# Performance work log

Measured on AMD Instinct MI355X. Metric: run time of the kernel, lower is better.

## Reference

```python
import jax, jax.numpy as jnp
import numpy as np

CUTOFFS = [20000, 40000, 200000, 267735]
CUTOFF_ENDS = [0] + CUTOFFS
DIMS = [1024, 256, 64, 16]  # d_embed // div_val**i


def setup_inputs() -> dict:
    key = jax.random.key(0)
    ks = jax.random.split(key, 20)
    def rn(k, shape):
        return jax.random.normal(k, shape, dtype=jnp.float32) * 0.02
    inp = {}
    inp["hidden"] = jax.random.normal(ks[0], (64, 8, 1024), dtype=jnp.float32)
    inp["target"] = jax.random.randint(ks[1], (64, 8), 0, 267735)
    inp["cluster_weight"] = rn(ks[2], (3, 1024))
    inp["cluster_bias"] = jnp.zeros((3,), jnp.float32)
    for i in range(4):
        n = CUTOFF_ENDS[i + 1] - CUTOFF_ENDS[i]
        inp[f"W{i}"] = rn(ks[3 + 3 * i], (n, DIMS[i]))
        inp[f"b{i}"] = jnp.zeros((n,), jnp.float32)
        inp[f"P{i}"] = rn(ks[4 + 3 * i], (DIMS[i], 1024))
    return inp


def _logit(h, W, b, P):
    # h: [s, b, d_proj]; P: [d_emb_i, d_proj]; W: [n_i, d_emb_i]
    y = jnp.einsum('ibd,ed->ibe', h, P)
    return jnp.einsum('ibe,ne->ibn', y, W) + b


def reference(hidden, target, cluster_weight, cluster_bias,
              W0, b0, P0, W1, b1, P1, W2, b2, P2, W3, b3, P3):
    Ws = [W0, W1, W2, W3]
    bs = [b0, b1, b2, b3]
    Ps = [P0, P1, P2, P3]

    # head cluster: real head tokens + cluster logits appended
    head_W = jnp.concatenate([W0, cluster_weight], axis=0)   # [20003, 1024]
    head_b = jnp.concatenate([b0, cluster_bias], axis=0)
    head_lp = jax.nn.log_softmax(_logit(hidden, head_W, head_b, P0), axis=-1)

    outs = [head_lp[..., :CUTOFFS[0]]]
    loss = jnp.zeros(target.shape, jnp.float32)

    mask = (target >= 0) & (target < CUTOFFS[0])
    ct = jnp.clip(target, 0, CUTOFFS[0] - 1)
    cur = jnp.take_along_axis(head_lp, ct[..., None], axis=-1)[..., 0]
    loss = jnp.where(mask, cur, loss)

    for i in range(1, 4):
        l_idx, r_idx = CUTOFF_ENDS[i], CUTOFF_ENDS[i + 1]
        tail_lp = jax.nn.log_softmax(_logit(hidden, Ws[i], bs[i], Ps[i]), axis=-1)
        # joint log-prob = cluster log-prob + within-cluster log-prob
        lp_i = head_lp[..., CUTOFFS[0] + i - 1, None] + tail_lp
        outs.append(lp_i)
        mask = (target >= l_idx) & (target < r_idx)
        ct = jnp.clip(target - l_idx, 0, r_idx - l_idx - 1)
        cur = jnp.take_along_axis(lp_i, ct[..., None], axis=-1)[..., 0]
        loss = jnp.where(mask, cur, loss)

    out = jnp.concatenate(outs, axis=-1)  # [s, b, vocab]
    loss = jnp.mean(-loss)                # return_mean=True
    return out, loss
```

## Files before the change

### kernel.cpp

```cpp
#include <hip/hip_runtime.h>


typedef __bf16 bf16x8 __attribute__((ext_vector_type(8)));
typedef float  f32x4  __attribute__((ext_vector_type(4)));

#define NEG_HUGE (-3.402823466e38f)

__device__ __forceinline__ unsigned short f2bf(float x) {
  unsigned int u = __float_as_uint(x);
  u = (u + 0x7fffu + ((u >> 16) & 1u)) >> 16;
  return (unsigned short)u;
}
__device__ __forceinline__ float bf2f(unsigned short h) {
  return __uint_as_float(((unsigned int)h) << 16);
}
__device__ __forceinline__ void mergeMS(float& m, float& s, float mo, float so) {
  float mn = fmaxf(m, mo);
  s = s * __expf(m - mn) + so * __expf(mo - mn);
  m = mn;
}

__global__ __launch_bounds__(256) void convert_h_kernel(
    const float* __restrict__ h, unsigned short* __restrict__ o) {
  int i = (blockIdx.x * 256 + threadIdx.x) * 4;
  float4 v = *reinterpret_cast<const float4*>(h + i);
  uint2 u;
  u.x = (unsigned int)f2bf(v.x) | ((unsigned int)f2bf(v.y) << 16);
  u.y = (unsigned int)f2bf(v.z) | ((unsigned int)f2bf(v.w) << 16);
  *reinterpret_cast<uint2*>(o + i) = u;
}

struct CvtDesc {
  const float* src[7];
  unsigned short* dst[7];
  int n4[7];
  int blk0[8];
};

__global__ __launch_bounds__(256) void convert_w_kernel(CvtDesc d) {
  int b = blockIdx.x, seg = 0;
  while (seg < 6 && b >= d.blk0[seg + 1]) ++seg;
  const float* __restrict__ s = d.src[seg];
  unsigned short* __restrict__ o = d.dst[seg];
  const int n4 = d.n4[seg];
  int base = (b - d.blk0[seg]) * 1024 + threadIdx.x;
#pragma unroll
  for (int i = 0; i < 4; ++i) {
    int v = base + i * 256;
    if (v < n4) {
      float4 x = reinterpret_cast<const float4*>(s)[v];
      uint2 u;
      u.x = (unsigned int)f2bf(x.x) | ((unsigned int)f2bf(x.y) << 16);
      u.y = (unsigned int)f2bf(x.z) | ((unsigned int)f2bf(x.w) << 16);
      reinterpret_cast<uint2*>(o)[v] = u;
    }
  }
}

__global__ __launch_bounds__(256) void convert_w3_kernel(
    const float* __restrict__ s, unsigned short* __restrict__ o) {
  int t = blockIdx.x * 256 + threadIdx.x;
  int row = t >> 2, j = t & 3;
  if (row >= 67735) return;
  uint4 u = make_uint4(0u, 0u, 0u, 0u);
  if (j < 2) {
    float4 a = reinterpret_cast<const float4*>(s)[row * 4 + j * 2];
    float4 b = reinterpret_cast<const float4*>(s)[row * 4 + j * 2 + 1];
    u.x = (unsigned int)f2bf(a.x) | ((unsigned int)f2bf(a.y) << 16);
    u.y = (unsigned int)f2bf(a.z) | ((unsigned int)f2bf(a.w) << 16);
    u.z = (unsigned int)f2bf(b.x) | ((unsigned int)f2bf(b.y) << 16);
    u.w = (unsigned int)f2bf(b.z) | ((unsigned int)f2bf(b.w) << 16);
  }
  reinterpret_cast<uint4*>(o)[row * 4 + j] = u;
}

template <bool SOFTMAX>
__global__ __launch_bounds__(256) void gemm_reg_kernel(
    const unsigned short* __restrict__ A, int lda, int K,
    const unsigned short* __restrict__ Bh, int ldb,
    const float* __restrict__ bias, int N,
    float* __restrict__ outF, long long ldo,
    unsigned short* __restrict__ outH, int ldh,
    float* __restrict__ partials, int nChunks) {
  __shared__ float red[64][4][2];
  const int tid = threadIdx.x;
  const int lane = tid & 63, w = tid >> 6;
  const int q = lane >> 4, l15 = lane & 15;
  const int row0 = blockIdx.x * 64;
  const int colBase = blockIdx.y * 256;

  const char* Ac = (const char*)A;
  const char* Bc = (const char*)Bh;
  int colg[4];
  unsigned aoff[4], boff[4];
#pragma unroll
  for (int nb = 0; nb < 4; ++nb) {
    colg[nb] = colBase + w * 64 + nb * 16 + l15;
    int cl = colg[nb] < N ? colg[nb] : N - 1;
    boff[nb] = (unsigned)((cl * ldb + q * 8) * 2);
  }
#pragma unroll
  for (int mb = 0; mb < 4; ++mb)
    aoff[mb] = (unsigned)(((row0 + mb * 16 + l15) * lda + q * 8) * 2);

  f32x4 acc[4][4];
#pragma unroll
  for (int i = 0; i < 4; ++i)
#pragma unroll
    for (int j = 0; j < 4; ++j) acc[i][j] = (f32x4){0.f, 0.f, 0.f, 0.f};

  for (int k = 0; k < K; k += 32) {
    bf16x8 fa[4], fb[4];
#pragma unroll
    for (int mb = 0; mb < 4; ++mb)
      fa[mb] = *reinterpret_cast<const bf16x8*>(Ac + aoff[mb] + 2 * k);
#pragma unroll
    for (int nb = 0; nb < 4; ++nb)
      fb[nb] = *reinterpret_cast<const bf16x8*>(Bc + boff[nb] + 2 * k);
#pragma unroll
    for (int mb = 0; mb < 4; ++mb)
#pragma unroll
      for (int nb = 0; nb < 4; ++nb)
        acc[mb][nb] = __builtin_amdgcn_mfma_f32_16x16x32_bf16(
            fa[mb], fb[nb], acc[mb][nb], 0, 0, 0);
  }

  if (SOFTMAX) {
    float bv[4];
#pragma unroll
    for (int nb = 0; nb < 4; ++nb) bv[nb] = (colg[nb] < N) ? bias[colg[nb]] : 0.f;
#pragma unroll
    for (int mb = 0; mb < 4; ++mb)
#pragma unroll
      for (int nb = 0; nb < 4; ++nb)
#pragma unroll
        for (int r = 0; r < 4; ++r) acc[mb][nb][r] += bv[nb];
#pragma unroll
    for (int mb = 0; mb < 4; ++mb)
#pragma unroll
      for (int nb = 0; nb < 4; ++nb)
        if (colg[nb] < N) {
#pragma unroll
          for (int r = 0; r < 4; ++r) {
            int rowg = row0 + mb * 16 + q * 4 + r;
            outF[(size_t)rowg * ldo + colg[nb]] = acc[mb][nb][r];
          }
        }
#pragma unroll
    for (int mb = 0; mb < 4; ++mb) {
#pragma unroll
      for (int r = 0; r < 4; ++r) {
        float mx = NEG_HUGE, s = 0.f;
#pragma unroll
        for (int nb = 0; nb < 4; ++nb)
          if (colg[nb] < N) mx = fmaxf(mx, acc[mb][nb][r]);
#pragma unroll
        for (int nb = 0; nb < 4; ++nb)
          if (colg[nb] < N) s += __expf(acc[mb][nb][r] - mx);
        for (int off = 1; off < 16; off <<= 1) {
          float mo = __shfl_xor(mx, off);
          float so = __shfl_xor(s, off);
          mergeMS(mx, s, mo, so);
        }
        if (l15 == 0) {
          red[mb * 16 + q * 4 + r][w][0] = mx;
          red[mb * 16 + q * 4 + r][w][1] = s;
        }
      }
    }
    __syncthreads();
    if (tid < 64) {
      float m = red[tid][0][0], s = red[tid][0][1];
#pragma unroll
      for (int ww = 1; ww < 4; ++ww) mergeMS(m, s, red[tid][ww][0], red[tid][ww][1]);
      size_t pi = ((size_t)(row0 + tid) * nChunks + blockIdx.y) * 2;
      partials[pi] = m;
      partials[pi + 1] = s;
    }
  } else {
#pragma unroll
    for (int mb = 0; mb < 4; ++mb)
#pragma unroll
      for (int nb = 0; nb < 4; ++nb)
        if (colg[nb] < ldh) {
#pragma unroll
          for (int r = 0; r < 4; ++r) {
            int rowg = row0 + mb * 16 + q * 4 + r;
            outH[(size_t)rowg * ldh + colg[nb]] =
                (colg[nb] < N) ? f2bf(acc[mb][nb][r]) : (unsigned short)0;
          }
        }
  }
}

template <int KS>
__global__ __launch_bounds__(256) void gemm_reg_mloop_kernel(
    const unsigned short* __restrict__ A, int lda,
    const unsigned short* __restrict__ Bh, int ldb,
    const float* __restrict__ bias, int N,
    float* __restrict__ outF, long long ldo,
    float* __restrict__ partials, int nChunks) {
  __shared__ float red[64][4][2];
  const int tid = threadIdx.x;
  const int lane = tid & 63, w = tid >> 6;
  const int q = lane >> 4, l15 = lane & 15;
  const int colBase = blockIdx.x * 256;

  const char* Ac = (const char*)A;
  const char* Bc = (const char*)Bh;
  int colg[4];
  float bv[4];
  bf16x8 fbr[KS][4];
#pragma unroll
  for (int nb = 0; nb < 4; ++nb) {
    colg[nb] = colBase + w * 64 + nb * 16 + l15;
    int cl = colg[nb] < N ? colg[nb] : N - 1;
    bv[nb] = (colg[nb] < N) ? bias[colg[nb]] : 0.f;
#pragma unroll
    for (int s = 0; s < KS; ++s)
      fbr[s][nb] = *reinterpret_cast<const bf16x8*>(
          Bc + (size_t)((cl * ldb + s * 32 + q * 8) * 2));
  }

  for (int m = 0; m < 8; ++m) {
    const int row0 = m * 64;
    f32x4 acc[4][4];
#pragma unroll
    for (int i = 0; i < 4; ++i)
#pragma unroll
      for (int j = 0; j < 4; ++j) acc[i][j] = (f32x4){0.f, 0.f, 0.f, 0.f};
#pragma unroll
    for (int s = 0; s < KS; ++s) {
      bf16x8 fa[4];
#pragma unroll
      for (int mb = 0; mb < 4; ++mb)
        fa[mb] = *reinterpret_cast<const bf16x8*>(
            Ac + (size_t)(((row0 + mb * 16 + l15) * lda + s * 32 + q * 8) * 2));
#pragma unroll
      for (int mb = 0; mb < 4; ++mb)
#pragma unroll
        for (int nb = 0; nb < 4; ++nb)
          acc[mb][nb] = __builtin_amdgcn_mfma_f32_16x16x32_bf16(
              fa[mb], fbr[s][nb], acc[mb][nb], 0, 0, 0);
    }
#pragma unroll
    for (int mb = 0; mb < 4; ++mb)
#pragma unroll
      for (int nb = 0; nb < 4; ++nb)
#pragma unroll
        for (int r = 0; r < 4; ++r) acc[mb][nb][r] += bv[nb];
#pragma unroll
    for (int mb = 0; mb < 4; ++mb)
#pragma unroll
      for (int nb = 0; nb < 4; ++nb)
        if (colg[nb] < N) {
#pragma unroll
          for (int r = 0; r < 4; ++r) {
            int rowg = row0 + mb * 16 + q * 4 + r;
            outF[(size_t)rowg * ldo + colg[nb]] = acc[mb][nb][r];
          }
        }
#pragma unroll
    for (int mb = 0; mb < 4; ++mb) {
#pragma unroll
      for (int r = 0; r < 4; ++r) {
        float mx = NEG_HUGE, s = 0.f;
#pragma unroll
        for (int nb = 0; nb < 4; ++nb)
          if (colg[nb] < N) mx = fmaxf(mx, acc[mb][nb][r]);
#pragma unroll
        for (int nb = 0; nb < 4; ++nb)
          if (colg[nb] < N) s += __expf(acc[mb][nb][r] - mx);
        for (int off = 1; off < 16; off <<= 1) {
          float mo = __shfl_xor(mx, off);
          float so = __shfl_xor(s, off);
          mergeMS(mx, s, mo, so);
        }
        if (l15 == 0) {
          red[mb * 16 + q * 4 + r][w][0] = mx;
          red[mb * 16 + q * 4 + r][w][1] = s;
        }
      }
    }
    __syncthreads();
    if (tid < 64) {
      float mm = red[tid][0][0], s = red[tid][0][1];
#pragma unroll
      for (int ww = 1; ww < 4; ++ww) mergeMS(mm, s, red[tid][ww][0], red[tid][ww][1]);
      size_t pi = ((size_t)(row0 + tid) * nChunks + blockIdx.x) * 2;
      partials[pi] = mm;
      partials[pi + 1] = s;
    }
    __syncthreads();
  }
}

constexpr int GBM = 64, GBN = 256, GBK = 64, GPK = GBK + 8;

template <bool SOFTMAX>
__global__ __launch_bounds__(256) void gemm_bt_kernel(
    const unsigned short* __restrict__ A, int lda, int K,
    const float* __restrict__ B, const float* __restrict__ bias, int N,
    float* __restrict__ outF, long long ldo,
    unsigned short* __restrict__ outH, int ldh,
    float* __restrict__ partials, int nChunks) {
  __shared__ unsigned short As[GBM][GPK];
  __shared__ unsigned short Bs[GBN][GPK];
  __shared__ float red[GBM][4][2];

  const int tid = threadIdx.x;
  const int lane = tid & 63, w = tid >> 6;
  const int q = lane >> 4, l15 = lane & 15;
  const int row0 = blockIdx.x * GBM;
  const int colBase = blockIdx.y * GBN;

  f32x4 acc[4][4];
#pragma unroll
  for (int i = 0; i < 4; ++i)
#pragma unroll
    for (int j = 0; j < 4; ++j) acc[i][j] = (f32x4){0.f, 0.f, 0.f, 0.f};

  for (int k0 = 0; k0 < K; k0 += GBK) {
    __syncthreads();
#pragma unroll
    for (int i = 0; i < 2; ++i) {
      int f = i * 2048 + tid * 8;
      int r = f >> 6, kk = f & 63;
      uint4 va = make_uint4(0u, 0u, 0u, 0u);
      if (k0 + kk < K)
        va = *reinterpret_cast<const uint4*>(A + (size_t)(row0 + r) * lda + k0 + kk);
      *reinterpret_cast<uint4*>(&As[r][kk]) = va;
    }
#pragma unroll
    for (int i = 0; i < 16; ++i) {
      int f = i * 1024 + tid * 4;
      int c = f >> 6, kk = f & 63;
      int col = colBase + c;
      float4 v = make_float4(0.f, 0.f, 0.f, 0.f);
      if (col < N && k0 + kk < K)
        v = *reinterpret_cast<const float4*>(B + (size_t)col * K + k0 + kk);
      uint2 u;
      u.x = (unsigned int)f2bf(v.x) | ((unsigned int)f2bf(v.y) << 16);
      u.y = (unsigned int)f2bf(v.z) | ((unsigned int)f2bf(v.w) << 16);
      *reinterpret_cast<uint2*>(&Bs[c][kk]) = u;
    }
    __syncthreads();
#pragma unroll
    for (int ks = 0; ks < GBK; ks += 32) {
      bf16x8 fa[4], fb[4];
#pragma unroll
      for (int mb = 0; mb < 4; ++mb)
        fa[mb] = *reinterpret_cast<const bf16x8*>(&As[mb * 16 + l15][ks + q * 8]);
#pragma unroll
      for (int nb = 0; nb < 4; ++nb)
        fb[nb] = *reinterpret_cast<const bf16x8*>(&Bs[w * 64 + nb * 16 + l15][ks + q * 8]);
#pragma unroll
      for (int mb = 0; mb < 4; ++mb)
#pragma unroll
        for (int nb = 0; nb < 4; ++nb)
          acc[mb][nb] = __builtin_amdgcn_mfma_f32_16x16x32_bf16(
              fa[mb], fb[nb], acc[mb][nb], 0, 0, 0);
    }
  }

  int colg[4];
#pragma unroll
  for (int nb = 0; nb < 4; ++nb) colg[nb] = colBase + w * 64 + nb * 16 + l15;

  if (SOFTMAX) {
    float bv[4];
#pragma unroll
    for (int nb = 0; nb < 4; ++nb) bv[nb] = (colg[nb] < N) ? bias[colg[nb]] : 0.f;
#pragma unroll
    for (int mb = 0; mb < 4; ++mb)
#pragma unroll
      for (int nb = 0; nb < 4; ++nb)
#pragma unroll
        for (int r = 0; r < 4; ++r) acc[mb][nb][r] += bv[nb];
#pragma unroll
    for (int mb = 0; mb < 4; ++mb)
#pragma unroll
      for (int nb = 0; nb < 4; ++nb)
        if (colg[nb] < N) {
#pragma unroll
          for (int r = 0; r < 4; ++r) {
            int rowg = row0 + mb * 16 + q * 4 + r;
            outF[(size_t)rowg * ldo + colg[nb]] = acc[mb][nb][r];
          }
        }
#pragma unroll
    for (int mb = 0; mb < 4; ++mb) {
#pragma unroll
      for (int r = 0; r < 4; ++r) {
        float mx = NEG_HUGE, s = 0.f;
#pragma unroll
        for (int nb = 0; nb < 4; ++nb)
          if (colg[nb] < N) mx = fmaxf(mx, acc[mb][nb][r]);
#pragma unroll
        for (int nb = 0; nb < 4; ++nb)
          if (colg[nb] < N) s += __expf(acc[mb][nb][r] - mx);
        for (int off = 1; off < 16; off <<= 1) {
          float mo = __shfl_xor(mx, off);
          float so = __shfl_xor(s, off);
          mergeMS(mx, s, mo, so);
        }
        if (l15 == 0) {
          red[mb * 16 + q * 4 + r][w][0] = mx;
          red[mb * 16 + q * 4 + r][w][1] = s;
        }
      }
    }
    __syncthreads();
    if (tid < 64) {
      float m = red[tid][0][0], s = red[tid][0][1];
#pragma unroll
      for (int ww = 1; ww < 4; ++ww) mergeMS(m, s, red[tid][ww][0], red[tid][ww][1]);
      size_t pi = ((size_t)(row0 + tid) * nChunks + blockIdx.y) * 2;
      partials[pi] = m;
      partials[pi + 1] = s;
    }
  } else {
#pragma unroll
    for (int mb = 0; mb < 4; ++mb)
#pragma unroll
      for (int nb = 0; nb < 4; ++nb)
        if (colg[nb] < N) {
#pragma unroll
          for (int r = 0; r < 4; ++r) {
            int rowg = row0 + mb * 16 + q * 4 + r;
            outH[(size_t)rowg * ldh + colg[nb]] = f2bf(acc[mb][nb][r]);
          }
        }
  }
}

__global__ __launch_bounds__(192) void cluster_kernel(
    const unsigned short* __restrict__ Y0, const float* __restrict__ CW,
    const float* __restrict__ CB, float* __restrict__ CL) {
  int row = blockIdx.x;
  int w = threadIdx.x >> 6, lane = threadIdx.x & 63;
  float s = 0.f;
  for (int k = lane; k < 1024; k += 64)
    s += bf2f(Y0[row * 1024 + k]) * CW[w * 1024 + k];
  for (int off = 32; off > 0; off >>= 1) s += __shfl_xor(s, off);
  if (lane == 0) CL[row * 3 + w] = s + CB[w];
}

__global__ __launch_bounds__(128) void reduce_stats_kernel(
    const float* __restrict__ part, const float* __restrict__ CL,
    float* __restrict__ stats) {
  const int nch[4] = {79, 79, 625, 265};
  const long long poff[4] = {0, 80896, 161792, 801792};
  int row = blockIdx.x >> 2, b = blockIdx.x & 3;
  const float* p = part + poff[b] + (long long)row * nch[b] * 2;
  float m = NEG_HUGE, s = 0.f;
  for (int j = threadIdx.x; j < nch[b]; j += 128) mergeMS(m, s, p[j * 2], p[j * 2 + 1]);
  for (int off = 1; off < 64; off <<= 1) {
    float mo = __shfl_xor(m, off);
    float so = __shfl_xor(s, off);
    mergeMS(m, s, mo, so);
  }
  __shared__ float sm[2][2];
  int w = threadIdx.x >> 6;
  if ((threadIdx.x & 63) == 0) { sm[w][0] = m; sm[w][1] = s; }
  __syncthreads();
  if (threadIdx.x == 0) {
    mergeMS(m, s, sm[1][0], sm[1][1]);
    if (b == 0)
      for (int c = 0; c < 3; ++c) mergeMS(m, s, CL[row * 3 + c], 1.f);
    stats[(row * 4 + b) * 2] = m;
    stats[(row * 4 + b) * 2 + 1] = logf(s);
  }
}

__global__ __launch_bounds__(256) void normalize_kernel(
    float* __restrict__ out, const float* __restrict__ stats,
    const float* __restrict__ CL) {
  const int row = blockIdx.x;
  const float s0 = stats[row * 8 + 0] + stats[row * 8 + 1];
  const float s1 = stats[(row * 4 + 1) * 2] + stats[(row * 4 + 1) * 2 + 1]
                   - (CL[row * 3 + 0] - s0);
  const float s2 = stats[(row * 4 + 2) * 2] + stats[(row * 4 + 2) * 2 + 1]
                   - (CL[row * 3 + 1] - s0);
  const float s3 = stats[(row * 4 + 3) * 2] + stats[(row * 4 + 3) * 2 + 1]
                   - (CL[row * 3 + 2] - s0);
  float* op = out + (size_t)row * 267735LL;
  const int lead = row & 3;
  const int NV = 66933;
  float4* vp = reinterpret_cast<float4*>(op + lead);

  int vbase = blockIdx.y * 1024 + threadIdx.x;
#pragma unroll
  for (int i = 0; i < 4; ++i) {
    int v = vbase + i * 256;
    if (v < NV) {
      float4 x = vp[v];
      int c0 = lead + v * 4;
      x.x -= (c0     < 20000) ? s0 : (c0     < 40000) ? s1 : (c0     < 200000) ? s2 : s3;
      x.y -= (c0 + 1 < 20000) ? s0 : (c0 + 1 < 40000) ? s1 : (c0 + 1 < 200000) ? s2 : s3;
      x.z -= (c0 + 2 < 20000) ? s0 : (c0 + 2 < 40000) ? s1 : (c0 + 2 < 200000) ? s2 : s3;
      x.w -= (c0 + 3 < 20000) ? s0 : (c0 + 3 < 40000) ? s1 : (c0 + 3 < 200000) ? s2 : s3;
      vp[v] = x;
    }
  }
  if (blockIdx.y == 0 && threadIdx.x == 0) {
    for (int c = 0; c < lead; ++c) op[c] -= s0;
    for (int c = lead + NV * 4; c < 267735; ++c) op[c] -= s3;
  }
}

__global__ __launch_bounds__(512) void loss_kernel(
    const float* __restrict__ out, const int* __restrict__ target,
    float* __restrict__ lossOut) {
  __shared__ float sm[512];
  int t = threadIdx.x;
  sm[t] = out[(size_t)t * 267735 + target[t]];
  __syncthreads();
  for (int s = 256; s > 0; s >>= 1) {
    if (t < s) sm[t] += sm[t + s];
    __syncthreads();
  }
  if (t == 0) lossOut[0] = -sm[0] / 512.f;
}

extern "C" void kernel_launch(void* const* d_in, const int* in_sizes, int n_in,
                              void* d_out, int out_size, void* d_ws, size_t ws_size,
                              hipStream_t stream) {
  const float* hidden = (const float*)d_in[0];
  const int* target = (const int*)d_in[1];
  const float* CW = (const float*)d_in[2];
  const float* CB = (const float*)d_in[3];
  const float* W[4] = {(const float*)d_in[4], (const float*)d_in[7],
                       (const float*)d_in[10], (const float*)d_in[13]};
  const float* Bb[4] = {(const float*)d_in[5], (const float*)d_in[8],
                        (const float*)d_in[11], (const float*)d_in[14]};
  const float* P[4] = {(const float*)d_in[6], (const float*)d_in[9],
                       (const float*)d_in[12], (const float*)d_in[15]};

  char* ws = (char*)d_ws;
  unsigned short* hbf = (unsigned short*)(ws + 0);
  unsigned short* Y[4] = {(unsigned short*)(ws + 1048576),
                          (unsigned short*)(ws + 2097152),
                          (unsigned short*)(ws + 2359296),
                          (unsigned short*)(ws + 2424832)};
  float* CL = (float*)(ws + 2457600);
  float* stats = (float*)(ws + 2463744);
  float* part = (float*)(ws + 2480128);

  const unsigned long long WBF = 6772736ull;
  unsigned short* Wb[4] = {(unsigned short*)(ws + WBF),
                           (unsigned short*)(ws + WBF + 40960000ull),
                           (unsigned short*)(ws + WBF + 51200000ull),
                           (unsigned short*)(ws + WBF + 71680000ull)};
  unsigned short* Pb[4] = {(unsigned short*)(ws + WBF + 76015040ull),
                           (unsigned short*)(ws + WBF + 78112192ull),
                           (unsigned short*)(ws + WBF + 78636480ull),
                           (unsigned short*)(ws + WBF + 78767552ull)};
  const bool BH = (ws_size >= WBF + 78800320ull);

  float* out = (float*)d_out;
  const int dims[4] = {1024, 256, 64, 16};
  const int nvoc[4] = {20000, 20000, 160000, 67735};
  const int colOff[4] = {0, 20000, 40000, 200000};
  const int nch[4] = {79, 79, 625, 265};
  const long long poffF[4] = {0, 80896, 161792, 801792};

  convert_h_kernel<<<512, 256, 0, stream>>>(hidden, hbf);

  if (BH) {
    CvtDesc d;
    const float* srcs[7] = {W[0], W[1], W[2], P[0], P[1], P[2], P[3]};
    unsigned short* dsts[7] = {Wb[0], Wb[1], Wb[2], Pb[0], Pb[1], Pb[2], Pb[3]};
    const int n4s[7] = {5120000, 1280000, 2560000, 262144, 65536, 16384, 4096};
    const int blk0s[8] = {0, 5000, 6250, 8750, 9006, 9070, 9086, 9090};
    for (int i = 0; i < 7; ++i) { d.src[i] = srcs[i]; d.dst[i] = dsts[i]; d.n4[i] = n4s[i]; }
    for (int i = 0; i < 8; ++i) d.blk0[i] = blk0s[i];
    convert_w_kernel<<<9090, 256, 0, stream>>>(d);
    convert_w3_kernel<<<1059, 256, 0, stream>>>(W[3], Wb[3]);

    for (int i = 0; i < 4; ++i) {
      dim3 g(8, (dims[i] + 255) / 256);
      gemm_reg_kernel<false><<<g, 256, 0, stream>>>(
          hbf, 1024, 1024, Pb[i], 1024, nullptr, dims[i],
          nullptr, 0, Y[i], (i == 3 ? 32 : dims[i]), nullptr, 0);
    }
    cluster_kernel<<<512, 192, 0, stream>>>(Y[0], CW, CB, CL);

    for (int i = 0; i < 2; ++i) {
      dim3 g(8, nch[i]);
      gemm_reg_kernel<true><<<g, 256, 0, stream>>>(
          Y[i], dims[i], dims[i], Wb[i], dims[i], Bb[i], nvoc[i],
          out + colOff[i], 267735LL, nullptr, 0, part + poffF[i], nch[i]);
    }
    gemm_reg_mloop_kernel<2><<<625, 256, 0, stream>>>(
        Y[2], 64, Wb[2], 64, Bb[2], 160000,
        out + 40000, 267735LL, part + poffF[2], 625);
    gemm_reg_mloop_kernel<1><<<265, 256, 0, stream>>>(
        Y[3], 32, Wb[3], 32, Bb[3], 67735,
        out + 200000, 267735LL, part + poffF[3], 265);
  } else {
    for (int i = 0; i < 4; ++i) {
      dim3 g(8, (dims[i] + 255) / 256);
      gemm_bt_kernel<false><<<g, 256, 0, stream>>>(
          hbf, 1024, 1024, P[i], nullptr, dims[i],
          nullptr, 0, Y[i], dims[i], nullptr, 0);
    }
    cluster_kernel<<<512, 192, 0, stream>>>(Y[0], CW, CB, CL);
    for (int i = 0; i < 4; ++i) {
      dim3 g(8, nch[i]);
      gemm_bt_kernel<true><<<g, 256, 0, stream>>>(
          Y[i], dims[i], dims[i], W[i], Bb[i], nvoc[i],
          out + colOff[i], 267735LL, nullptr, 0, part + poffF[i], nch[i]);
    }
  }

  reduce_stats_kernel<<<512 * 4, 128, 0, stream>>>(part, CL, stats);
  dim3 gn(512, 66);
  normalize_kernel<<<gn, 256, 0, stream>>>(out, stats, CL);
  loss_kernel<<<1, 512, 0, stream>>>(out, target, out + 137080320LL);
}
```

Before: 1.318 ms.

## Recompute small-dim tail logits after stats to write normalized output directly

For the two cheap tail clusters (dims 64 and 16), the GEMM now runs twice: a first pass computes only softmax partial stats without storing logits, and after the stats reduction a second pass recomputes the logits and writes them already normalized. The normalize pass is then limited to the first 40000 columns. This removes a full read-modify-write of roughly 228k columns per row of the output, trading it for redundant low-K GEMM compute and an extra launch.

```diff
diff --git a/kernel.cpp b/kernel.cpp
--- a/kernel.cpp
+++ b/kernel.cpp
@@ -193,14 +193,16 @@
   }
 }
 
-template <int KS>
+template <int KS, int MODE>
 __global__ __launch_bounds__(256) void gemm_reg_mloop_kernel(
     const unsigned short* __restrict__ A, int lda,
     const unsigned short* __restrict__ Bh, int ldb,
     const float* __restrict__ bias, int N,
     float* __restrict__ outF, long long ldo,
-    float* __restrict__ partials, int nChunks) {
+    float* __restrict__ partials, int nChunks,
+    const float* __restrict__ stats, const float* __restrict__ CL, int bucket) {
   __shared__ float red[64][4][2];
+  __shared__ float subs[64];
   const int tid = threadIdx.x;
   const int lane = tid & 63, w = tid >> 6;
   const int q = lane >> 4, l15 = lane & 15;
@@ -224,6 +226,15 @@
 
   for (int m = 0; m < 8; ++m) {
     const int row0 = m * 64;
+    if (MODE == 3) {
+      if (tid < 64) {
+        int row = row0 + tid;
+        float s0 = stats[row * 8] + stats[row * 8 + 1];
+        subs[tid] = stats[(row * 4 + bucket) * 2] + stats[(row * 4 + bucket) * 2 + 1]
+                    - (CL[row * 3 + (bucket - 1)] - s0);
+      }
+      __syncthreads();
+    }
     f32x4 acc[4][4];
 #pragma unroll
     for (int i = 0; i < 4; ++i)
@@ -249,49 +260,54 @@
       for (int nb = 0; nb < 4; ++nb)
 #pragma unroll
         for (int r = 0; r < 4; ++r) acc[mb][nb][r] += bv[nb];
-#pragma unroll
-    for (int mb = 0; mb < 4; ++mb)
-#pragma unroll
-      for (int nb = 0; nb < 4; ++nb)
-        if (colg[nb] < N) {
-#pragma unroll
-          for (int r = 0; r < 4; ++r) {
-            int rowg = row0 + mb * 16 + q * 4 + r;
-            outF[(size_t)rowg * ldo + colg[nb]] = acc[mb][nb][r];
+
+    if (MODE == 3) {
+#pragma unroll
+      for (int mb = 0; mb < 4; ++mb)
+#pragma unroll
+        for (int nb = 0; nb < 4; ++nb)
+          if (colg[nb] < N) {
+#pragma unroll
+            for (int r = 0; r < 4; ++r) {
+              int rl = mb * 16 + q * 4 + r;
+              outF[(size_t)(row0 + rl) * ldo + colg[nb]] = acc[mb][nb][r] - subs[rl];
+            }
           }
-        }
-#pragma unroll
-    for (int mb = 0; mb < 4; ++mb) {
-#pragma unroll
-      for (int r = 0; r < 4; ++r) {
-        float mx = NEG_HUGE, s = 0.f;
-#pragma unroll
-        for (int nb = 0; nb < 4; ++nb)
-          if (colg[nb] < N) mx = fmaxf(mx, acc[mb][nb][r]);
-#pragma unroll
-        for (int nb = 0; nb < 4; ++nb)
-          if (colg[nb] < N) s += __expf(acc[mb][nb][r] - mx);
-        for (int off = 1; off < 16; off <<= 1) {
-          float mo = __shfl_xor(mx, off);
-          float so = __shfl_xor(s, off);
-          mergeMS(mx, s, mo, so);
-        }
-        if (l15 == 0) {
-          red[mb * 16 + q * 4 + r][w][0] = mx;
-          red[mb * 16 + q * 4 + r][w][1] = s;
+      __syncthreads();
+    } else {
+#pragma unroll
+      for (int mb = 0; mb < 4; ++mb) {
+#pragma unroll
+        for (int r = 0; r < 4; ++r) {
+          float mx = NEG_HUGE, s = 0.f;
+#pragma unroll
+          for (int nb = 0; nb < 4; ++nb)
+            if (colg[nb] < N) mx = fmaxf(mx, acc[mb][nb][r]);
+#pragma unroll
+          for (int nb = 0; nb < 4; ++nb)
+            if (colg[nb] < N) s += __expf(acc[mb][nb][r] - mx);
+          for (int off = 1; off < 16; off <<= 1) {
+            float mo = __shfl_xor(mx, off);
+            float so = __shfl_xor(s, off);
+            mergeMS(mx, s, mo, so);
+          }
+          if (l15 == 0) {
+            red[mb * 16 + q * 4 + r][w][0] = mx;
+            red[mb * 16 + q * 4 + r][w][1] = s;
+          }
         }
       }
-    }
-    __syncthreads();
-    if (tid < 64) {
-      float mm = red[tid][0][0], s = red[tid][0][1];
-#pragma unroll
-      for (int ww = 1; ww < 4; ++ww) mergeMS(mm, s, red[tid][ww][0], red[tid][ww][1]);
-      size_t pi = ((size_t)(row0 + tid) * nChunks + blockIdx.x) * 2;
-      partials[pi] = mm;
-      partials[pi + 1] = s;
-    }
-    __syncthreads();
+      __syncthreads();
+      if (tid < 64) {
+        float mm = red[tid][0][0], s = red[tid][0][1];
+#pragma unroll
+        for (int ww = 1; ww < 4; ++ww) mergeMS(mm, s, red[tid][ww][0], red[tid][ww][1]);
+        size_t pi = ((size_t)(row0 + tid) * nChunks + blockIdx.x) * 2;
+        partials[pi] = mm;
+        partials[pi + 1] = s;
+      }
+      __syncthreads();
+    }
   }
 }
 
@@ -475,7 +491,7 @@
 
 __global__ __launch_bounds__(256) void normalize_kernel(
     float* __restrict__ out, const float* __restrict__ stats,
-    const float* __restrict__ CL) {
+    const float* __restrict__ CL, int maxcol) {
   const int row = blockIdx.x;
   const float s0 = stats[row * 8 + 0] + stats[row * 8 + 1];
   const float s1 = stats[(row * 4 + 1) * 2] + stats[(row * 4 + 1) * 2 + 1]
@@ -486,7 +502,7 @@
                    - (CL[row * 3 + 2] - s0);
   float* op = out + (size_t)row * 267735LL;
   const int lead = row & 3;
-  const int NV = 66933;
+  const int NV = (maxcol - lead) >> 2;
   float4* vp = reinterpret_cast<float4*>(op + lead);
 
   int vbase = blockIdx.y * 1024 + threadIdx.x;
@@ -505,7 +521,8 @@
   }
   if (blockIdx.y == 0 && threadIdx.x == 0) {
     for (int c = 0; c < lead; ++c) op[c] -= s0;
-    for (int c = lead + NV * 4; c < 267735; ++c) op[c] -= s3;
+    for (int c = lead + NV * 4; c < maxcol; ++c)
+      op[c] -= (c < 20000) ? s0 : (c < 40000) ? s1 : (c < 200000) ? s2 : s3;
   }
 }
 
@@ -592,12 +609,24 @@
           Y[i], dims[i], dims[i], Wb[i], dims[i], Bb[i], nvoc[i],
           out + colOff[i], 267735LL, nullptr, 0, part + poffF[i], nch[i]);
     }
-    gemm_reg_mloop_kernel<2><<<625, 256, 0, stream>>>(
+    gemm_reg_mloop_kernel<2, 2><<<625, 256, 0, stream>>>(
         Y[2], 64, Wb[2], 64, Bb[2], 160000,
-        out + 40000, 267735LL, part + poffF[2], 625);
-    gemm_reg_mloop_kernel<1><<<265, 256, 0, stream>>>(
+        nullptr, 0, part + poffF[2], 625, nullptr, nullptr, 2);
+    gemm_reg_mloop_kernel<1, 2><<<265, 256, 0, stream>>>(
         Y[3], 32, Wb[3], 32, Bb[3], 67735,
-        out + 200000, 267735LL, part + poffF[3], 265);
+        nullptr, 0, part + poffF[3], 265, nullptr, nullptr, 3);
+
+    reduce_stats_kernel<<<512 * 4, 128, 0, stream>>>(part, CL, stats);
+
+    gemm_reg_mloop_kernel<2, 3><<<625, 256, 0, stream>>>(
+        Y[2], 64, Wb[2], 64, Bb[2], 160000,
+        out + 40000, 267735LL, nullptr, 625, stats, CL, 2);
+    gemm_reg_mloop_kernel<1, 3><<<265, 256, 0, stream>>>(
+        Y[3], 32, Wb[3], 32, Bb[3], 67735,
+        out + 200000, 267735LL, nullptr, 265, stats, CL, 3);
+
+    dim3 gn(512, 10);
+    normalize_kernel<<<gn, 256, 0, stream>>>(out, stats, CL, 40000);
   } else {
     for (int i = 0; i < 4; ++i) {
       dim3 g(8, (dims[i] + 255) / 256);
@@ -612,10 +641,10 @@
           Y[i], dims[i], dims[i], W[i], Bb[i], nvoc[i],
           out + colOff[i], 267735LL, nullptr, 0, part + poffF[i], nch[i]);
     }
-  }
-
-  reduce_stats_kernel<<<512 * 4, 128, 0, stream>>>(part, CL, stats);
-  dim3 gn(512, 66);
-  normalize_kernel<<<gn, 256, 0, stream>>>(out, stats, CL);
+    reduce_stats_kernel<<<512 * 4, 128, 0, stream>>>(part, CL, stats);
+    dim3 gn(512, 66);
+    normalize_kernel<<<gn, 256, 0, stream>>>(out, stats, CL, 267735);
+  }
+
   loss_kernel<<<1, 512, 0, stream>>>(out, target, out + 137080320LL);
 }
```

After: 1.180 ms. 1.12x faster.
